# Performance work log

Measured on AMD Instinct MI355X. Metric: run time of the kernel, lower is better.

The kernel has to match this reference:

```python
import jax, jax.numpy as jnp
import numpy as np

N, E, F_IN, H, G, OUT = 50000, 800000, 64, 128, 64, 16


def setup_inputs() -> dict:
    key = jax.random.key(0)
    ks = jax.random.split(key, 16)
    x = jax.random.normal(ks[0], (N, F_IN), dtype=jnp.float32)
    edge_index = jax.random.randint(ks[1], (2, E), 0, N, dtype=jnp.int64)
    edge_attr = jax.random.normal(ks[2], (E,), dtype=jnp.float32)
    batch = jnp.sort(jax.random.randint(ks[3], (N,), 0, G, dtype=jnp.int64))
    d_in = 2 * F_IN  # NaN mask doubles the feature dim
    s = lambda f: 1.0 / np.sqrt(f)
    W0 = jax.random.uniform(ks[4], (d_in, H), jnp.float32, -s(d_in), s(d_in))
    b0 = jnp.zeros((H,), jnp.float32)
    W1 = jax.random.uniform(ks[5], (H, H), jnp.float32, -s(H), s(H))
    b1 = jnp.zeros((H,), jnp.float32)
    W2 = jax.random.uniform(ks[6], (H, H), jnp.float32, -s(H), s(H))
    b2 = jnp.zeros((H,), jnp.float32)
    bn_gamma = 1.0 + 0.1 * jax.random.normal(ks[7], (H,), jnp.float32)
    bn_beta = 0.1 * jax.random.normal(ks[8], (H,), jnp.float32)
    bn_mean = 0.1 * jax.random.normal(ks[9], (H,), jnp.float32)
    bn_var = jnp.abs(1.0 + 0.1 * jax.random.normal(ks[10], (H,), jnp.float32))
    mW1 = jax.random.uniform(ks[11], (H, H), jnp.float32, -s(H), s(H))
    mb1 = jax.random.uniform(ks[12], (H,), jnp.float32, -s(H), s(H))
    mW2 = jax.random.uniform(ks[13], (H, OUT), jnp.float32, -s(H), s(H))
    mb2 = jax.random.uniform(ks[14], (OUT,), jnp.float32, -s(H), s(H))
    return dict(x=x, edge_index=edge_index, edge_attr=edge_attr, batch=batch,
                W0=W0, b0=b0, W1=W1, b1=b1, W2=W2, b2=b2,
                bn_gamma=bn_gamma, bn_beta=bn_beta, bn_mean=bn_mean, bn_var=bn_var,
                mW1=mW1, mb1=mb1, mW2=mW2, mb2=mb2)


def _gcn_conv(h_in, row, col, w, W, b, n):
    # PyG GCNConv with edge_weight, add_self_loops=True (self-loop weight 1)
    h = h_in @ W                                   # [N, H]
    deg = jax.ops.segment_sum(w, col, num_segments=n) + 1.0
    dinv = jnp.where(deg > 0, jax.lax.rsqrt(deg), 0.0)
    norm = dinv[row] * w * dinv[col]               # [E]
    agg = jax.ops.segment_sum(norm[:, None] * h[row], col, num_segments=n)
    agg = agg + (dinv * dinv)[:, None] * h         # self-loop contribution
    return agg + b


def _bn_eval(h, gamma, beta, mean, var, eps=1e-5):
    return (h - mean) * jax.lax.rsqrt(var + eps) * gamma + beta


def reference(x, edge_index, edge_attr, batch,
              W0, b0, W1, b1, W2, b2,
              bn_gamma, bn_beta, bn_mean, bn_var,
              mW1, mb1, mW2, mb2):
    n = x.shape[0]
    # handle_nan_features: zero NaNs and append binary NaN-mask channels
    nan_mask = jnp.isnan(x).astype(x.dtype)
    h = jnp.concatenate([jnp.nan_to_num(x, nan=0.0), nan_mask], axis=-1)
    w = jnp.abs(jnp.nan_to_num(edge_attr.reshape(-1), nan=0.0))
    row, col = edge_index[0], edge_index[1]
    for (W, b) in ((W0, b0), (W1, b1)):
        h = _gcn_conv(h, row, col, w, W, b, n)
        h = _bn_eval(h, bn_gamma, bn_beta, bn_mean, bn_var)
        h = jax.nn.relu(h)
        # dropout: identity in eval mode
    h = _gcn_conv(h, row, col, w, W2, b2, n)
    # global mean pool over graphs
    sums = jax.ops.segment_sum(h, batch, num_segments=G)
    cnts = jax.ops.segment_sum(jnp.ones((n,), h.dtype), batch, num_segments=G)
    g = sums / jnp.maximum(cnts, 1.0)[:, None]     # [G, H]
    g = jax.nn.gelu(g @ mW1 + mb1, approximate=False)
    return g @ mW2 + mb2                            # [G, OUT]
```

## Files before the change

### kernel.cpp

```cpp
#include <hip/hip_runtime.h>
#include <hip/hip_bf16.h>
#include <stdint.h>

#define HD 128
#define GD 64
#define OUTD 16
#define NR 16

typedef unsigned short u16;
typedef __attribute__((ext_vector_type(8))) short short8;
typedef __attribute__((ext_vector_type(4))) float f32x4;

__device__ __forceinline__ float bf2f(u16 u) {
  union { uint32_t i; float f; } v; v.i = ((uint32_t)u) << 16; return v.f;
}
__device__ __forceinline__ u16 f2bf(float f) {
  union { __hip_bfloat16 h; u16 u; } v; v.h = __float2bfloat16(f); return v.u;
}

__global__ __launch_bounds__(256)
void convert_count_k(const int* __restrict__ ei, const int* __restrict__ bt,
                     int2* __restrict__ eidx, int* __restrict__ b32,
                     int* __restrict__ cntR, int* __restrict__ rank,
                     int E, int N) {
  __shared__ int s_is64;
  if (threadIdx.x == 0) {
    int all0 = 1;
    for (int k = 1; k < 128; k += 2) all0 &= (ei[k] == 0);
    s_is64 = all0;
  }
  __syncthreads();
  int is64 = s_is64;
  int i = blockIdx.x * 256 + threadIdx.x;
  if (i < E) {
    int r = is64 ? ei[2 * i] : ei[i];
    int c = is64 ? ei[2 * (E + i)] : ei[E + i];
    r = (r < 0) ? 0 : (r >= N ? N - 1 : r);
    c = (c < 0) ? 0 : (c >= N ? N - 1 : c);
    eidx[i] = make_int2(r, c);
    int k = blockIdx.x & (NR - 1);
    rank[i] = atomicAdd(&cntR[k * N + c], 1);
  }
  if (i < N) {
    int v = is64 ? bt[2 * i] : bt[i];
    b32[i] = (v < 0) ? 0 : (v >= GD ? GD - 1 : v);
  }
}

__global__ void scan1_k(const int* __restrict__ cntR, int* __restrict__ offs,
                        int* __restrict__ bsum, int Np, int N) {
  __shared__ int s[1024];
  int i = blockIdx.x * 1024 + threadIdx.x;
  int v = 0;
  if (i < Np) {
#pragma unroll
    for (int k = 0; k < NR; ++k) v += cntR[k * N + i];
  }
  s[threadIdx.x] = v;
  __syncthreads();
  for (int off = 1; off < 1024; off <<= 1) {
    int t = (threadIdx.x >= off) ? s[threadIdx.x - off] : 0;
    __syncthreads();
    s[threadIdx.x] += t;
    __syncthreads();
  }
  if (i < Np) offs[i] = s[threadIdx.x] - v;
  if (threadIdx.x == 1023) bsum[blockIdx.x] = s[1023];
}
__global__ void scan2_k(int* bsum, int nb) {
  if (threadIdx.x == 0 && blockIdx.x == 0) {
    int sum = 0;
    for (int i = 0; i < nb; ++i) { int v = bsum[i]; bsum[i] = sum; sum += v; }
  }
}
__global__ void scan3_k(int* __restrict__ offs, const int* __restrict__ bsum,
                        int Np, int E) {
  int i = blockIdx.x * 256 + threadIdx.x;
  if (i < Np) offs[i] = offs[i] + bsum[i >> 10];
  if (i == 0) offs[Np] = E;
}

__global__ void cursR_k(const int* __restrict__ offs, const int* __restrict__ cntR,
                        int* __restrict__ cursR, int N) {
  int n = blockIdx.x * 256 + threadIdx.x;
  if (n >= N) return;
  int run = offs[n];
#pragma unroll
  for (int k = 0; k < NR; ++k) { cursR[k * N + n] = run; run += cntR[k * N + n]; }
}

__global__ __launch_bounds__(256)
void fill_k(const int2* __restrict__ eidx, const float* __restrict__ ea,
            const int* __restrict__ cursR, const int* __restrict__ rank,
            int2* __restrict__ csc, int E, int N) {
  int e = blockIdx.x * 256 + threadIdx.x;
  if (e >= E) return;
  int k = blockIdx.x & (NR - 1);
  int2 rc = eidx[e];
  float a = ea[e];
  float w = isnan(a) ? 0.f : fabsf(a);
  int p = cursR[k * N + rc.y] + rank[e];
  csc[p] = make_int2(rc.x, __float_as_int(w));
}

__global__ void deg_k(const int* __restrict__ offs, const int2* __restrict__ csc,
                      float* __restrict__ dinv, int N) {
  int n = blockIdx.x * 256 + threadIdx.x;
  if (n >= N) return;
  int p = offs[n], pe = offs[n + 1];
  float s = 0.f;
  for (; p < pe; ++p) s += __int_as_float(csc[p].y);
  dinv[n] = rsqrtf(s + 1.0f);
}

__global__ void normcsc_k(const int* __restrict__ offs, int2* __restrict__ csc,
                          const float* __restrict__ dinv, int N) {
  int n = blockIdx.x * 256 + threadIdx.x;
  if (n >= N) return;
  float dc = dinv[n];
  int p = offs[n], pe = offs[n + 1];
  for (; p < pe; ++p) {
    int2 v = csc[p];
    v.y = __float_as_int(dinv[v.x] * __int_as_float(v.y) * dc);
    csc[p] = v;
  }
}

__global__ void convw3_k(const float* __restrict__ W0, const float* __restrict__ W1,
                         const float* __restrict__ W2, u16* __restrict__ Wt) {
  int i = blockIdx.x * 256 + threadIdx.x;
  if (i >= 3 * HD * HD) return;
  int l = i / (HD * HD);
  int r = i - l * (HD * HD);
  int n = r >> 7, k = r & 127;
  const float* W = (l == 0) ? W0 : (l == 1) ? W1 : W2;
  Wt[i] = f2bf(W[k * HD + n]);
}

__device__ __forceinline__ void gemm_core(const u16* sw, const short8* afr,
                                          int m, int qd, int orow,
                                          u16* __restrict__ B, int N) {
#pragma unroll
  for (int c = 0; c < 8; ++c) {
    f32x4 acc = {0.f, 0.f, 0.f, 0.f};
    const int n = c * 16 + m;
#pragma unroll
    for (int s = 0; s < 4; ++s) {
      short8 bfr = *(const short8*)(sw + n * 136 + 32 * s + 8 * qd);
      acc = __builtin_amdgcn_mfma_f32_16x16x32_bf16(afr[s], bfr, acc, 0, 0, 0);
    }
#pragma unroll
    for (int r = 0; r < 4; ++r) {
      int rr = orow + r;
      if (rr < N) B[(size_t)rr * HD + n] = f2bf(acc[r]);
    }
  }
}

__device__ __forceinline__ void stage_w(const u16* __restrict__ Wt, u16* sw, int t) {
  const uint32_t* src = (const uint32_t*)Wt;
  uint32_t* dst = (uint32_t*)sw;
#pragma unroll
  for (int k = 0; k < 32; ++k) {
    int q = t + k * 256;
    int r = q >> 6;
    int u = q & 63;
    dst[r * 68 + u] = src[r * 64 + u];
  }
}

__global__ __launch_bounds__(256)
void gemm0_k(const float* __restrict__ x, const u16* __restrict__ Wt,
             u16* __restrict__ B, int N) {
  __shared__ u16 sw[128 * 136];
  const int t = threadIdx.x;
  stage_w(Wt, sw, t);
  __syncthreads();
  const int w = t >> 6;
  const int lane = t & 63;
  const int m = lane & 15;
  const int qd = lane >> 4;
  const int arow = blockIdx.x * 64 + w * 16 + m;
  short8 afr[4];
  if (arow < N) {
    const float* xp = x + (size_t)arow * 64;
    float v0[8], v1[8];
    *(float4*)&v0[0] = *(const float4*)(xp + 8 * qd);
    *(float4*)&v0[4] = *(const float4*)(xp + 8 * qd + 4);
    *(float4*)&v1[0] = *(const float4*)(xp + 32 + 8 * qd);
    *(float4*)&v1[4] = *(const float4*)(xp + 32 + 8 * qd + 4);
#pragma unroll
    for (int j = 0; j < 8; ++j) {
      bool n0 = isnan(v0[j]), n1 = isnan(v1[j]);
      afr[0][j] = (short)f2bf(n0 ? 0.f : v0[j]);
      afr[1][j] = (short)f2bf(n1 ? 0.f : v1[j]);
      afr[2][j] = (short)(n0 ? 0x3F80 : 0);
      afr[3][j] = (short)(n1 ? 0x3F80 : 0);
    }
  } else {
    short8 z = {0, 0, 0, 0, 0, 0, 0, 0};
#pragma unroll
    for (int s = 0; s < 4; ++s) afr[s] = z;
  }
  const int orow = blockIdx.x * 64 + w * 16 + qd * 4;
  gemm_core(sw, afr, m, qd, orow, B, N);
}

__global__ __launch_bounds__(256)
void gemm_k(const u16* __restrict__ A, const u16* __restrict__ Wt,
            u16* __restrict__ B, int N) {
  __shared__ u16 sw[128 * 136];
  const int t = threadIdx.x;
  stage_w(Wt, sw, t);
  __syncthreads();
  const int w = t >> 6;
  const int lane = t & 63;
  const int m = lane & 15;
  const int qd = lane >> 4;
  const int arow = blockIdx.x * 64 + w * 16 + m;
  short8 afr[4];
  if (arow < N) {
    const short8* ap = (const short8*)(A + (size_t)arow * HD);
#pragma unroll
    for (int s = 0; s < 4; ++s) afr[s] = ap[4 * s + qd];
  } else {
    short8 z = {0, 0, 0, 0, 0, 0, 0, 0};
#pragma unroll
    for (int s = 0; s < 4; ++s) afr[s] = z;
  }
  const int orow = blockIdx.x * 64 + w * 16 + qd * 4;
  gemm_core(sw, afr, m, qd, orow, B, N);
}

__global__ __launch_bounds__(256)
void aggregate_k(const int* __restrict__ offs, const int2* __restrict__ csc,
                 const u16* __restrict__ B, const float* __restrict__ dinv,
                 const float* __restrict__ bias, const float* __restrict__ gamma,
                 const float* __restrict__ beta, const float* __restrict__ mean,
                 const float* __restrict__ var, int do_bn,
                 u16* __restrict__ A, int N) {
  int tid = blockIdx.x * 256 + threadIdx.x;
  int n = tid >> 4;
  if (n >= N) return;
  int f8 = (tid & 15) << 3;
  float d = dinv[n];
  float d2 = d * d;
  float acc[8];
  short8 bu = *(const short8*)(B + (size_t)n * HD + f8);
  float4 bi0 = *(const float4*)(bias + f8);
  float4 bi1 = *(const float4*)(bias + f8 + 4);
#pragma unroll
  for (int j = 0; j < 8; ++j) acc[j] = d2 * bf2f((u16)bu[j]);
  acc[0] += bi0.x; acc[1] += bi0.y; acc[2] += bi0.z; acc[3] += bi0.w;
  acc[4] += bi1.x; acc[5] += bi1.y; acc[6] += bi1.z; acc[7] += bi1.w;

  int p = offs[n], pe = offs[n + 1];
  for (; p + 3 < pe; p += 4) {
    int2 e0 = csc[p], e1 = csc[p + 1], e2 = csc[p + 2], e3 = csc[p + 3];
    short8 h0 = *(const short8*)(B + (size_t)e0.x * HD + f8);
    short8 h1 = *(const short8*)(B + (size_t)e1.x * HD + f8);
    short8 h2 = *(const short8*)(B + (size_t)e2.x * HD + f8);
    short8 h3 = *(const short8*)(B + (size_t)e3.x * HD + f8);
    float w0 = __int_as_float(e0.y), w1 = __int_as_float(e1.y);
    float w2 = __int_as_float(e2.y), w3 = __int_as_float(e3.y);
#pragma unroll
    for (int j = 0; j < 8; ++j) {
      acc[j] += w0 * bf2f((u16)h0[j]) + w1 * bf2f((u16)h1[j])
              + w2 * bf2f((u16)h2[j]) + w3 * bf2f((u16)h3[j]);
    }
  }
  for (; p < pe; ++p) {
    int2 e0 = csc[p];
    float w0 = __int_as_float(e0.y);
    short8 h0 = *(const short8*)(B + (size_t)e0.x * HD + f8);
#pragma unroll
    for (int j = 0; j < 8; ++j) acc[j] += w0 * bf2f((u16)h0[j]);
  }
  if (do_bn) {
#pragma unroll
    for (int j = 0; j < 8; ++j) {
      float s = gamma[f8 + j] * rsqrtf(var[f8 + j] + 1e-5f);
      float v = (acc[j] - mean[f8 + j]) * s + beta[f8 + j];
      acc[j] = v > 0.f ? v : 0.f;
    }
  }
  short8 o;
#pragma unroll
  for (int j = 0; j < 8; ++j) o[j] = (short)f2bf(acc[j]);
  *(short8*)(A + (size_t)n * HD + f8) = o;
}

__device__ __forceinline__ int seg_lower_bound(const int* b32, int N, int b) {
  int lo = 0, hi = N;
  while (lo < hi) {
    int mid = (lo + hi) >> 1;
    if (b32[mid] < b) lo = mid + 1; else hi = mid;
  }
  return lo;
}

__global__ __launch_bounds__(128)
void pool1_k(const u16* __restrict__ A, const int* __restrict__ b32,
             float* __restrict__ sums, int N) {
  __shared__ int sb[2];
  int b = blockIdx.y;
  if (threadIdx.x == 0) sb[0] = seg_lower_bound(b32, N, b);
  if (threadIdx.x == 1) sb[1] = seg_lower_bound(b32, N, b + 1);
  __syncthreads();
  int s = sb[0], e = sb[1];
  int len = e - s;
  if (len <= 0) return;
  int nch = gridDim.x;
  int ch = (len + nch - 1) / nch;
  int lo = s + blockIdx.x * ch;
  int hi = lo + ch; if (hi > e) hi = e;
  if (lo >= hi) return;
  int j = threadIdx.x;
  float a0 = 0.f, a1 = 0.f, a2 = 0.f, a3 = 0.f;
  int n = lo;
  for (; n + 3 < hi; n += 4) {
    a0 += bf2f(A[(size_t)(n + 0) * HD + j]);
    a1 += bf2f(A[(size_t)(n + 1) * HD + j]);
    a2 += bf2f(A[(size_t)(n + 2) * HD + j]);
    a3 += bf2f(A[(size_t)(n + 3) * HD + j]);
  }
  for (; n < hi; ++n) a0 += bf2f(A[(size_t)n * HD + j]);
  unsafeAtomicAdd(&sums[b * HD + j], (a0 + a1) + (a2 + a3));
}

__global__ __launch_bounds__(128)
void mlp_k(const float* __restrict__ sums, const int* __restrict__ b32,
           const float* __restrict__ mW1, const float* __restrict__ mb1,
           const float* __restrict__ mW2, const float* __restrict__ mb2,
           float* __restrict__ out, int N) {
  __shared__ float sg[128];
  __shared__ float st[128];
  __shared__ int sb[2];
  int b = blockIdx.x, j = threadIdx.x;
  if (j == 0) sb[0] = seg_lower_bound(b32, N, b);
  if (j == 1) sb[1] = seg_lower_bound(b32, N, b + 1);
  __syncthreads();
  int cnt = sb[1] - sb[0];
  float inv = 1.0f / (float)(cnt > 0 ? cnt : 1);
  sg[j] = sums[b * HD + j] * inv;
  __syncthreads();
  float s = mb1[j];
#pragma unroll 4
  for (int i = 0; i < 128; ++i) s += sg[i] * mW1[i * 128 + j];
  float ge = 0.5f * s * (1.0f + erff(s * 0.70710678118654752f));
  st[j] = ge;
  __syncthreads();
  if (j < OUTD) {
    float o = mb2[j];
#pragma unroll 4
    for (int k = 0; k < 128; ++k) o += st[k] * mW2[k * OUTD + j];
    out[b * OUTD + j] = o;
  }
}

extern "C" void kernel_launch(void* const* d_in, const int* in_sizes, int n_in,
                              void* d_out, int out_size, void* d_ws, size_t ws_size,
                              hipStream_t stream) {
  const float* x   = (const float*)d_in[0];
  const int* ei    = (const int*)d_in[1];
  const float* ea  = (const float*)d_in[2];
  const int* bt    = (const int*)d_in[3];
  const float* W0  = (const float*)d_in[4];
  const float* b0  = (const float*)d_in[5];
  const float* W1  = (const float*)d_in[6];
  const float* b1  = (const float*)d_in[7];
  const float* W2  = (const float*)d_in[8];
  const float* b2  = (const float*)d_in[9];
  const float* bng = (const float*)d_in[10];
  const float* bnb = (const float*)d_in[11];
  const float* bnm = (const float*)d_in[12];
  const float* bnv = (const float*)d_in[13];
  const float* mW1 = (const float*)d_in[14];
  const float* mb1 = (const float*)d_in[15];
  const float* mW2 = (const float*)d_in[16];
  const float* mb2 = (const float*)d_in[17];
  float* out = (float*)d_out;

  const int N = in_sizes[0] / 64;
  const int E = in_sizes[2];

  char* ws = (char*)d_ws;
  size_t NB2 = (size_t)N * HD * 2;
  u16* A       = (u16*)(ws);
  u16* B       = (u16*)(ws + NB2);
  char* q      = ws + 2 * NB2;
  u16* Wt      = (u16*)q;              q += (size_t)3 * HD * HD * 2;
  int2* csc    = (int2*)q;             q += (size_t)E * 8;
  int2* eidx   = (int2*)q;             q += (size_t)E * 8;
  int*  rank   = (int*)q;              q += (size_t)E * 4;
  float* dinv  = (float*)q;            q += (size_t)N * 4;
  int*   cntR  = (int*)q;              q += (size_t)NR * N * 4;
  int*   cursR = (int*)q;              q += (size_t)NR * N * 4;
  int*   offs  = (int*)q;              q += (size_t)(N + 2) * 4;
  int*   b32   = (int*)q;              q += (size_t)N * 4;
  int*   bsum  = (int*)q;              q += 64 * 4;
  float* sums  = (float*)q;            q += GD * HD * 4;

  dim3 blk(256);
  int gE  = (E + 255) / 256;
  int gN  = (N + 255) / 256;
  int nb1024 = (N + 1023) / 1024;

  hipMemsetAsync(cntR, 0, (size_t)NR * N * 4, stream);
  hipMemsetAsync(sums, 0, (size_t)GD * HD * 4, stream);
  convert_count_k<<<gE, blk, 0, stream>>>(ei, bt, eidx, b32, cntR, rank, E, N);
  scan1_k<<<nb1024, 1024, 0, stream>>>(cntR, offs, bsum, N, N);
  scan2_k<<<1, 64, 0, stream>>>(bsum, nb1024);
  scan3_k<<<gN, blk, 0, stream>>>(offs, bsum, N, E);
  cursR_k<<<gN, blk, 0, stream>>>(offs, cntR, cursR, N);
  fill_k<<<gE, blk, 0, stream>>>(eidx, ea, cursR, rank, csc, E, N);
  deg_k<<<gN, blk, 0, stream>>>(offs, csc, dinv, N);
  normcsc_k<<<gN, blk, 0, stream>>>(offs, csc, dinv, N);
  convw3_k<<<(3 * HD * HD + 255) / 256, blk, 0, stream>>>(W0, W1, W2, Wt);

  int gGemm = (N + 63) / 64;
  int gAgg  = (N * 16 + 255) / 256;

  gemm0_k<<<gGemm, 256, 0, stream>>>(x, Wt, B, N);
  aggregate_k<<<gAgg, blk, 0, stream>>>(offs, csc, B, dinv, b0,
                                        bng, bnb, bnm, bnv, 1, A, N);
  gemm_k<<<gGemm, 256, 0, stream>>>(A, Wt + HD * HD, B, N);
  aggregate_k<<<gAgg, blk, 0, stream>>>(offs, csc, B, dinv, b1,
                                        bng, bnb, bnm, bnv, 1, A, N);
  gemm_k<<<gGemm, 256, 0, stream>>>(A, Wt + 2 * HD * HD, B, N);
  aggregate_k<<<gAgg, blk, 0, stream>>>(offs, csc, B, dinv, b2,
                                        bng, bnb, bnm, bnv, 0, A, N);

  dim3 pgrid(16, GD);
  pool1_k<<<pgrid, 128, 0, stream>>>(A, b32, sums, N);
  mlp_k<<<GD, 128, 0, stream>>>(sums, b32, mW1, mb1, mW2, mb2, out, N);
}
```

Before: 337.9 us.

## Fold symmetric degree normalization into GEMM epilogue and drop edge-norm pass

Rewrites the GCN normalization algebraically: the GEMM output rows are pre-scaled by dinv[row], and aggregation multiplies by dinv[col] at the end. This removes the per-edge normcsc pass that gathered dinv for every edge. It also merges the scan3 and cursor kernels, merges the two memsets into one by placing their buffers next to each other, unrolls the aggregation gather loop to 8 edges, and doubles the pooling grid. The edge weights in csc are now raw |w|, and scaling the bf16-stored features before rounding slightly changes rounding behaviour.

```diff
diff --git a/kernel.cpp b/kernel.cpp
--- a/kernel.cpp
+++ b/kernel.cpp
@@ -73,20 +73,18 @@
     for (int i = 0; i < nb; ++i) { int v = bsum[i]; bsum[i] = sum; sum += v; }
   }
 }
-__global__ void scan3_k(int* __restrict__ offs, const int* __restrict__ bsum,
-                        int Np, int E) {
-  int i = blockIdx.x * 256 + threadIdx.x;
-  if (i < Np) offs[i] = offs[i] + bsum[i >> 10];
-  if (i == 0) offs[Np] = E;
-}
-
-__global__ void cursR_k(const int* __restrict__ offs, const int* __restrict__ cntR,
-                        int* __restrict__ cursR, int N) {
+__global__ void scan3curs_k(int* __restrict__ offs, const int* __restrict__ bsum,
+                            const int* __restrict__ cntR, int* __restrict__ cursR,
+                            int Np, int E, int N) {
   int n = blockIdx.x * 256 + threadIdx.x;
-  if (n >= N) return;
-  int run = offs[n];
-#pragma unroll
-  for (int k = 0; k < NR; ++k) { cursR[k * N + n] = run; run += cntR[k * N + n]; }
+  if (n < Np) {
+    int o = offs[n] + bsum[n >> 10];
+    offs[n] = o;
+    int run = o;
+#pragma unroll
+    for (int k = 0; k < NR; ++k) { cursR[k * N + n] = run; run += cntR[k * N + n]; }
+  }
+  if (n == 0) offs[Np] = E;
 }
 
 __global__ __launch_bounds__(256)
@@ -113,19 +111,6 @@
   dinv[n] = rsqrtf(s + 1.0f);
 }
 
-__global__ void normcsc_k(const int* __restrict__ offs, int2* __restrict__ csc,
-                          const float* __restrict__ dinv, int N) {
-  int n = blockIdx.x * 256 + threadIdx.x;
-  if (n >= N) return;
-  float dc = dinv[n];
-  int p = offs[n], pe = offs[n + 1];
-  for (; p < pe; ++p) {
-    int2 v = csc[p];
-    v.y = __float_as_int(dinv[v.x] * __int_as_float(v.y) * dc);
-    csc[p] = v;
-  }
-}
-
 __global__ void convw3_k(const float* __restrict__ W0, const float* __restrict__ W1,
                          const float* __restrict__ W2, u16* __restrict__ Wt) {
   int i = blockIdx.x * 256 + threadIdx.x;
@@ -139,7 +124,11 @@
 
 __device__ __forceinline__ void gemm_core(const u16* sw, const short8* afr,
                                           int m, int qd, int orow,
+                                          const float* __restrict__ dinv,
                                           u16* __restrict__ B, int N) {
+  float dr[4];
+#pragma unroll
+  for (int r = 0; r < 4; ++r) dr[r] = (orow + r < N) ? dinv[orow + r] : 0.f;
 #pragma unroll
   for (int c = 0; c < 8; ++c) {
     f32x4 acc = {0.f, 0.f, 0.f, 0.f};
@@ -152,7 +141,7 @@
 #pragma unroll
     for (int r = 0; r < 4; ++r) {
       int rr = orow + r;
-      if (rr < N) B[(size_t)rr * HD + n] = f2bf(acc[r]);
+      if (rr < N) B[(size_t)rr * HD + n] = f2bf(dr[r] * acc[r]);
     }
   }
 }
@@ -171,7 +160,7 @@
 
 __global__ __launch_bounds__(256)
 void gemm0_k(const float* __restrict__ x, const u16* __restrict__ Wt,
-             u16* __restrict__ B, int N) {
+             const float* __restrict__ dinv, u16* __restrict__ B, int N) {
   __shared__ u16 sw[128 * 136];
   const int t = threadIdx.x;
   stage_w(Wt, sw, t);
@@ -203,12 +192,12 @@
     for (int s = 0; s < 4; ++s) afr[s] = z;
   }
   const int orow = blockIdx.x * 64 + w * 16 + qd * 4;
-  gemm_core(sw, afr, m, qd, orow, B, N);
+  gemm_core(sw, afr, m, qd, orow, dinv, B, N);
 }
 
 __global__ __launch_bounds__(256)
 void gemm_k(const u16* __restrict__ A, const u16* __restrict__ Wt,
-            u16* __restrict__ B, int N) {
+            const float* __restrict__ dinv, u16* __restrict__ B, int N) {
   __shared__ u16 sw[128 * 136];
   const int t = threadIdx.x;
   stage_w(Wt, sw, t);
@@ -229,7 +218,7 @@
     for (int s = 0; s < 4; ++s) afr[s] = z;
   }
   const int orow = blockIdx.x * 64 + w * 16 + qd * 4;
-  gemm_core(sw, afr, m, qd, orow, B, N);
+  gemm_core(sw, afr, m, qd, orow, dinv, B, N);
 }
 
 __global__ __launch_bounds__(256)
@@ -243,39 +232,45 @@
   int n = tid >> 4;
   if (n >= N) return;
   int f8 = (tid & 15) << 3;
-  float d = dinv[n];
-  float d2 = d * d;
   float acc[8];
   short8 bu = *(const short8*)(B + (size_t)n * HD + f8);
-  float4 bi0 = *(const float4*)(bias + f8);
-  float4 bi1 = *(const float4*)(bias + f8 + 4);
-#pragma unroll
-  for (int j = 0; j < 8; ++j) acc[j] = d2 * bf2f((u16)bu[j]);
-  acc[0] += bi0.x; acc[1] += bi0.y; acc[2] += bi0.z; acc[3] += bi0.w;
-  acc[4] += bi1.x; acc[5] += bi1.y; acc[6] += bi1.z; acc[7] += bi1.w;
+#pragma unroll
+  for (int j = 0; j < 8; ++j) acc[j] = bf2f((u16)bu[j]);
 
   int p = offs[n], pe = offs[n + 1];
-  for (; p + 3 < pe; p += 4) {
-    int2 e0 = csc[p], e1 = csc[p + 1], e2 = csc[p + 2], e3 = csc[p + 3];
+  for (; p + 7 < pe; p += 8) {
+    int2 e[8];
+    short8 h[8];
+#pragma unroll
+    for (int u = 0; u < 8; ++u) e[u] = csc[p + u];
+#pragma unroll
+    for (int u = 0; u < 8; ++u) h[u] = *(const short8*)(B + (size_t)e[u].x * HD + f8);
+#pragma unroll
+    for (int u = 0; u < 8; ++u) {
+      float w = __int_as_float(e[u].y);
+#pragma unroll
+      for (int j = 0; j < 8; ++j) acc[j] += w * bf2f((u16)h[u][j]);
+    }
+  }
+  for (; p + 1 < pe; p += 2) {
+    int2 e0 = csc[p], e1 = csc[p + 1];
     short8 h0 = *(const short8*)(B + (size_t)e0.x * HD + f8);
     short8 h1 = *(const short8*)(B + (size_t)e1.x * HD + f8);
-    short8 h2 = *(const short8*)(B + (size_t)e2.x * HD + f8);
-    short8 h3 = *(const short8*)(B + (size_t)e3.x * HD + f8);
     float w0 = __int_as_float(e0.y), w1 = __int_as_float(e1.y);
-    float w2 = __int_as_float(e2.y), w3 = __int_as_float(e3.y);
-#pragma unroll
-    for (int j = 0; j < 8; ++j) {
-      acc[j] += w0 * bf2f((u16)h0[j]) + w1 * bf2f((u16)h1[j])
-              + w2 * bf2f((u16)h2[j]) + w3 * bf2f((u16)h3[j]);
-    }
-  }
-  for (; p < pe; ++p) {
+#pragma unroll
+    for (int j = 0; j < 8; ++j)
+      acc[j] += w0 * bf2f((u16)h0[j]) + w1 * bf2f((u16)h1[j]);
+  }
+  if (p < pe) {
     int2 e0 = csc[p];
     float w0 = __int_as_float(e0.y);
     short8 h0 = *(const short8*)(B + (size_t)e0.x * HD + f8);
 #pragma unroll
     for (int j = 0; j < 8; ++j) acc[j] += w0 * bf2f((u16)h0[j]);
   }
+  float dn = dinv[n];
+#pragma unroll
+  for (int j = 0; j < 8; ++j) acc[j] = dn * acc[j] + bias[f8 + j];
   if (do_bn) {
 #pragma unroll
     for (int j = 0; j < 8; ++j) {
@@ -389,49 +384,46 @@
   u16* A       = (u16*)(ws);
   u16* B       = (u16*)(ws + NB2);
   char* q      = ws + 2 * NB2;
+  int*   cntR  = (int*)q;              q += (size_t)NR * N * 4;
+  float* sums  = (float*)q;            q += GD * HD * 4;
   u16* Wt      = (u16*)q;              q += (size_t)3 * HD * HD * 2;
   int2* csc    = (int2*)q;             q += (size_t)E * 8;
   int2* eidx   = (int2*)q;             q += (size_t)E * 8;
   int*  rank   = (int*)q;              q += (size_t)E * 4;
   float* dinv  = (float*)q;            q += (size_t)N * 4;
-  int*   cntR  = (int*)q;              q += (size_t)NR * N * 4;
   int*   cursR = (int*)q;              q += (size_t)NR * N * 4;
   int*   offs  = (int*)q;              q += (size_t)(N + 2) * 4;
   int*   b32   = (int*)q;              q += (size_t)N * 4;
   int*   bsum  = (int*)q;              q += 64 * 4;
-  float* sums  = (float*)q;            q += GD * HD * 4;
 
   dim3 blk(256);
   int gE  = (E + 255) / 256;
   int gN  = (N + 255) / 256;
   int nb1024 = (N + 1023) / 1024;
 
-  hipMemsetAsync(cntR, 0, (size_t)NR * N * 4, stream);
-  hipMemsetAsync(sums, 0, (size_t)GD * HD * 4, stream);
+  hipMemsetAsync(cntR, 0, (size_t)NR * N * 4 + (size_t)GD * HD * 4, stream);
   convert_count_k<<<gE, blk, 0, stream>>>(ei, bt, eidx, b32, cntR, rank, E, N);
   scan1_k<<<nb1024, 1024, 0, stream>>>(cntR, offs, bsum, N, N);
   scan2_k<<<1, 64, 0, stream>>>(bsum, nb1024);
-  scan3_k<<<gN, blk, 0, stream>>>(offs, bsum, N, E);
-  cursR_k<<<gN, blk, 0, stream>>>(offs, cntR, cursR, N);
+  scan3curs_k<<<gN, blk, 0, stream>>>(offs, bsum, cntR, cursR, N, E, N);
   fill_k<<<gE, blk, 0, stream>>>(eidx, ea, cursR, rank, csc, E, N);
   deg_k<<<gN, blk, 0, stream>>>(offs, csc, dinv, N);
-  normcsc_k<<<gN, blk, 0, stream>>>(offs, csc, dinv, N);
   convw3_k<<<(3 * HD * HD + 255) / 256, blk, 0, stream>>>(W0, W1, W2, Wt);
 
   int gGemm = (N + 63) / 64;
   int gAgg  = (N * 16 + 255) / 256;
 
-  gemm0_k<<<gGemm, 256, 0, stream>>>(x, Wt, B, N);
+  gemm0_k<<<gGemm, 256, 0, stream>>>(x, Wt, dinv, B, N);
   aggregate_k<<<gAgg, blk, 0, stream>>>(offs, csc, B, dinv, b0,
                                         bng, bnb, bnm, bnv, 1, A, N);
-  gemm_k<<<gGemm, 256, 0, stream>>>(A, Wt + HD * HD, B, N);
+  gemm_k<<<gGemm, 256, 0, stream>>>(A, Wt + HD * HD, dinv, B, N);
   aggregate_k<<<gAgg, blk, 0, stream>>>(offs, csc, B, dinv, b1,
                                         bng, bnb, bnm, bnv, 1, A, N);
-  gemm_k<<<gGemm, 256, 0, stream>>>(A, Wt + 2 * HD * HD, B, N);
+  gemm_k<<<gGemm, 256, 0, stream>>>(A, Wt + 2 * HD * HD, dinv, B, N);
   aggregate_k<<<gAgg, blk, 0, stream>>>(offs, csc, B, dinv, b2,
                                         bng, bnb, bnm, bnv, 0, A, N);
 
-  dim3 pgrid(16, GD);
+  dim3 pgrid(32, GD);
   pool1_k<<<pgrid, 128, 0, stream>>>(A, b32, sums, N);
   mlp_k<<<GD, 128, 0, stream>>>(sums, b32, mW1, mb1, mW2, mb2, out, N);
 }
```

After: 333.8 us. Within noise of the previous version (-1.2%).
